# Optimization experiments

Measured on AMD Instinct MI355X. Metric: run time of the kernel, lower is better.

Reference implementation:

```python
import jax, jax.numpy as jnp
import numpy as np

QUERY_DIM = 1024
CONTEXT_DIM = 1024
HEADS = 8
DIM_HEAD = 64
INNER = HEADS * DIM_HEAD  # 512
SCALE = DIM_HEAD ** -0.5


def setup_inputs() -> dict:
    key = jax.random.key(0)
    ks = jax.random.split(key, 7)
    B, N, M = 2, 2048, 2048
    x = jax.random.normal(ks[0], (B, N, QUERY_DIM), dtype=jnp.float32)
    context = jax.random.normal(ks[1], (B, M, CONTEXT_DIM), dtype=jnp.float32)
    # nn.Linear weights (stored as [out, in] in torch; we use [in, out] here)
    Wq = jax.random.normal(ks[2], (QUERY_DIM, INNER), dtype=jnp.float32) * (QUERY_DIM ** -0.5)
    Wk = jax.random.normal(ks[3], (CONTEXT_DIM, INNER), dtype=jnp.float32) * (CONTEXT_DIM ** -0.5)
    Wv = jax.random.normal(ks[4], (CONTEXT_DIM, INNER), dtype=jnp.float32) * (CONTEXT_DIM ** -0.5)
    Wo = jax.random.normal(ks[5], (INNER, QUERY_DIM), dtype=jnp.float32) * (INNER ** -0.5)
    bo = jax.random.normal(ks[6], (QUERY_DIM,), dtype=jnp.float32) * 0.01
    return {"x": x, "context": context, "Wq": Wq, "Wk": Wk, "Wv": Wv, "Wo": Wo, "bo": bo}


def reference(x, context, Wq, Wk, Wv, Wo, bo):
    B, N, _ = x.shape
    M = context.shape[1]
    # projections (no bias, matching nn.Linear(bias=False))
    q = (x @ Wq).reshape(B, N, HEADS, DIM_HEAD)          # b i h d
    k = (context @ Wk).reshape(B, M, HEADS, DIM_HEAD)    # b j h d
    v = (context @ Wv).reshape(B, M, HEADS, DIM_HEAD)    # b j h d
    # scores in fp32 (ATTN_PRECISION=='fp32' path)
    sim = jnp.einsum('bihd,bjhd->bhij', q.astype(jnp.float32), k.astype(jnp.float32)) * SCALE
    attn = jax.nn.softmax(sim, axis=-1).astype(v.dtype)  # b h i j
    out = jnp.einsum('bhij,bjhd->bihd', attn, v).reshape(B, N, INNER)
    return out @ Wo + bo  # dropout p=0.0 is identity
```

## Files before the change

kernel.cpp:

```cpp
#include <hip/hip_runtime.h>
#include <math.h>

typedef __bf16 bf16_t;
typedef __bf16 bf16x8 __attribute__((ext_vector_type(8)));
typedef __bf16 bf16x4 __attribute__((ext_vector_type(4)));
typedef float  f32x4  __attribute__((ext_vector_type(4)));

#define MFMA16(a, b, c) __builtin_amdgcn_mfma_f32_16x16x32_bf16((a), (b), (c), 0, 0, 0)

#define INNER   512
#define DHEAD   64
#define QSCALE  0.18033688f

__device__ __forceinline__ void g2l(const bf16_t* g, bf16_t* l) {
  __builtin_amdgcn_global_load_lds(
      (const __attribute__((address_space(1))) unsigned int*)g,
      (__attribute__((address_space(3))) unsigned int*)l, 16, 0, 0);
}

__global__ __launch_bounds__(256) void cvt_k(const float* __restrict__ x,
                                             const float* __restrict__ ctx,
                                             bf16_t* __restrict__ xb,
                                             bf16_t* __restrict__ cb) {
  const float* in = blockIdx.y ? ctx : x;
  bf16_t* out     = blockIdx.y ? cb  : xb;
  int i = blockIdx.x * 256 + threadIdx.x;
  float4 f = ((const float4*)in)[i];
  bf16x4 v = { (bf16_t)f.x, (bf16_t)f.y, (bf16_t)f.z, (bf16_t)f.w };
  ((bf16x4*)out)[i] = v;
}

__global__ __launch_bounds__(256) void wtrans_k(const float* __restrict__ Wq,
                                                const float* __restrict__ Wk,
                                                const float* __restrict__ Wv,
                                                const float* __restrict__ Wo,
                                                bf16_t* __restrict__ WqT,
                                                bf16_t* __restrict__ WkT,
                                                bf16_t* __restrict__ WvT,
                                                bf16_t* __restrict__ WoT) {
  int z = blockIdx.y;
  const float* W; bf16_t* WT; int K, N;
  if (z == 0)      { W = Wq; WT = WqT; K = 1024; N = 512; }
  else if (z == 1) { W = Wk; WT = WkT; K = 1024; N = 512; }
  else if (z == 2) { W = Wv; WT = WvT; K = 1024; N = 512; }
  else             { W = Wo; WT = WoT; K = 512;  N = 1024; }
  int tK = K >> 6;
  int bid = blockIdx.x;
  int kt = bid % tK, nt = bid / tK;
  int k0 = kt << 6, n0 = nt << 6;
  __shared__ float tile[64][65];
  for (int idx = threadIdx.x; idx < 4096; idx += 256) {
    int r = idx >> 6, c = idx & 63;
    tile[r][c] = W[(size_t)(k0 + r) * N + n0 + c];
  }
  __syncthreads();
  for (int idx = threadIdx.x; idx < 4096; idx += 256) {
    int r = idx >> 6, c = idx & 63;
    WT[(size_t)(n0 + r) * K + k0 + c] = (bf16_t)tile[c][r];
  }
}

__global__ __launch_bounds__(256) void vtrans_k(const bf16_t* __restrict__ Vb,
                                                bf16_t* __restrict__ Vt) {
  int m0 = blockIdx.x << 6;
  int bh = blockIdx.y;
  int b = bh >> 3, h = bh & 7;
  __shared__ bf16_t tile[64][65];
  for (int idx = threadIdx.x; idx < 4096; idx += 256) {
    int r = idx >> 6, c = idx & 63;
    tile[r][c] = Vb[(size_t)(b * 2048 + m0 + r) * INNER + h * DHEAD + c];
  }
  __syncthreads();
  for (int idx = threadIdx.x; idx < 4096; idx += 256) {
    int r = idx >> 6, c = idx & 63;
    Vt[((size_t)bh * 64 + r) * 2048 + m0 + c] = tile[c][r];
  }
}

__device__ __forceinline__ void gemm128(const bf16_t* __restrict__ A,
                                        const bf16_t* __restrict__ Bt,
                                        int K, int N, int row0, int n0, float scale,
                                        bf16_t* __restrict__ Cb, float* __restrict__ Cf,
                                        const float* __restrict__ bias) {
  __shared__ bf16_t As[128 * 40];
  __shared__ bf16_t Bs[128 * 40];
  const int tid = threadIdx.x;
  const int w = tid >> 6, lane = tid & 63, quad = lane >> 4, l16 = lane & 15;
  const int sr = tid >> 2, sc = (tid & 3) << 3;
  const bf16_t* ga = A  + (size_t)(row0 + sr) * K + sc;
  const bf16_t* gb = Bt + (size_t)(n0  + sr) * K + sc;

  f32x4 acc[4][4];
#pragma unroll
  for (int i = 0; i < 4; ++i)
#pragma unroll
    for (int j = 0; j < 4; ++j) acc[i][j] = f32x4{0.f, 0.f, 0.f, 0.f};

  int4 ra0 = *(const int4*)(ga);
  int4 ra1 = *(const int4*)(ga + (size_t)64 * K);
  int4 rb0 = *(const int4*)(gb);
  int4 rb1 = *(const int4*)(gb + (size_t)64 * K);

  const int mrow = (w & 1) << 6, ncol = (w >> 1) << 6;
  const int KT = K >> 5;
  for (int kt = 0; kt < KT; ++kt) {
    __syncthreads();
    *(int4*)&As[sr * 40 + sc]        = ra0;
    *(int4*)&As[(sr + 64) * 40 + sc] = ra1;
    *(int4*)&Bs[sr * 40 + sc]        = rb0;
    *(int4*)&Bs[(sr + 64) * 40 + sc] = rb1;
    __syncthreads();
    if (kt + 1 < KT) {
      int k0 = (kt + 1) << 5;
      ra0 = *(const int4*)(ga + k0);
      ra1 = *(const int4*)(ga + (size_t)64 * K + k0);
      rb0 = *(const int4*)(gb + k0);
      rb1 = *(const int4*)(gb + (size_t)64 * K + k0);
    }
    bf16x8 af[4], bfr[4];
#pragma unroll
    for (int i = 0; i < 4; ++i)
      af[i] = *(const bf16x8*)&As[(mrow + i * 16 + l16) * 40 + quad * 8];
#pragma unroll
    for (int j = 0; j < 4; ++j)
      bfr[j] = *(const bf16x8*)&Bs[(ncol + j * 16 + l16) * 40 + quad * 8];
#pragma unroll
    for (int i = 0; i < 4; ++i)
#pragma unroll
      for (int j = 0; j < 4; ++j)
        acc[i][j] = MFMA16(af[i], bfr[j], acc[i][j]);
  }
#pragma unroll
  for (int i = 0; i < 4; ++i) {
    int row = row0 + mrow + i * 16 + quad * 4;
#pragma unroll
    for (int j = 0; j < 4; ++j) {
      int col = n0 + ncol + j * 16 + l16;
#pragma unroll
      for (int r = 0; r < 4; ++r) {
        if (Cf) Cf[(size_t)(row + r) * N + col] = acc[i][j][r] + bias[col];
        else    Cb[(size_t)(row + r) * N + col] = (bf16_t)(acc[i][j][r] * scale);
      }
    }
  }
}

__global__ __launch_bounds__(256, 2) void gemm_qkv_k(const bf16_t* __restrict__ xb,
                                                     const bf16_t* __restrict__ cb,
                                                     const bf16_t* __restrict__ WqT,
                                                     const bf16_t* __restrict__ WkT,
                                                     const bf16_t* __restrict__ WvT,
                                                     bf16_t* __restrict__ Qb,
                                                     bf16_t* __restrict__ Kb,
                                                     bf16_t* __restrict__ Vb) {
  int z = blockIdx.z;
  const bf16_t* A  = (z == 0) ? xb : cb;
  const bf16_t* Bt = (z == 0) ? WqT : (z == 1) ? WkT : WvT;
  bf16_t* C        = (z == 0) ? Qb  : (z == 1) ? Kb  : Vb;
  float scale      = (z == 0) ? QSCALE : 1.0f;
  gemm128(A, Bt, 1024, 512, blockIdx.y * 128, blockIdx.x * 128, scale, C, nullptr, nullptr);
}

__global__ __launch_bounds__(256, 2) void gemm_out_k(const bf16_t* __restrict__ AO,
                                                     const bf16_t* __restrict__ WoT,
                                                     const float* __restrict__ bo,
                                                     float* __restrict__ out) {
  gemm128(AO, WoT, 512, 1024, blockIdx.y * 128, blockIdx.x * 128, 1.0f, nullptr, out, bo);
}

__global__ __launch_bounds__(256, 3) void attn_k(const bf16_t* __restrict__ Qb,
                                                 const bf16_t* __restrict__ Kb,
                                                 const bf16_t* __restrict__ Vt,
                                                 bf16_t* __restrict__ AO) {
  const int tid = threadIdx.x;
  const int w = tid >> 6, lane = tid & 63, quad = lane >> 4, l16 = lane & 15;
  const int qt = blockIdx.x;
  const int bh = blockIdx.y;
  const int b = bh >> 3, h = bh & 7;

  __shared__ bf16_t KsB[128 * 64];
  __shared__ bf16_t VsB[64 * 128];
  __shared__ bf16_t Ps[64 * 136];

  const int qrow = b * 2048 + qt * 64 + w * 16 + l16;
  const bf16_t* qptr = Qb + (size_t)qrow * INNER + h * DHEAD;
  bf16x8 bq[2];
  bq[0] = *(const bf16x8*)(qptr + quad * 8);
  bq[1] = *(const bf16x8*)(qptr + 32 + quad * 8);

  f32x4 o[4];
#pragma unroll
  for (int dt = 0; dt < 4; ++dt) o[dt] = f32x4{0.f, 0.f, 0.f, 0.f};
  float m_s = -__builtin_inff(), l_s = 0.f;

  const bf16_t* kbase  = Kb + ((size_t)b * 2048) * INNER + h * DHEAD;
  const bf16_t* vtbase = Vt + ((size_t)bh * 64) * 2048;

  const int krow_c = w * 32 + (lane >> 3);
  const int kcol_c = ((lane & 7) ^ (lane >> 3)) << 3;
  const int vrow_c = w * 16 + (lane >> 4);
  bf16_t* ksl = &KsB[w * 2048];
  bf16_t* vsl = &VsB[w * 2048];

  for (int kt = 0; kt < 16; ++kt) {
    __syncthreads();
#pragma unroll
    for (int p = 0; p < 4; ++p) {
      g2l(kbase + (size_t)(kt * 128 + krow_c + p * 8) * INNER + kcol_c,
          ksl + p * 512);
      int vlog = ((lane & 15) ^ ((p * 4 + (lane >> 4)) & 15)) << 3;
      g2l(vtbase + (size_t)(vrow_c + p * 4) * 2048 + kt * 128 + vlog,
          vsl + p * 512);
    }
    __syncthreads();

    f32x4 s[8];
#pragma unroll
    for (int jt = 0; jt < 8; ++jt) s[jt] = f32x4{0.f, 0.f, 0.f, 0.f};
#pragma unroll
    for (int jt = 0; jt < 8; ++jt) {
#pragma unroll
      for (int ks = 0; ks < 2; ++ks) {
        int phys = ((ks * 4 + quad) ^ (l16 & 7)) << 3;
        bf16x8 ak = *(const bf16x8*)&KsB[(jt * 16 + l16) * 64 + phys];
        s[jt] = MFMA16(ak, bq[ks], s[jt]);
      }
    }

    float mx = -__builtin_inff();
#pragma unroll
    for (int jt = 0; jt < 8; ++jt) {
      float a = fmaxf(fmaxf(s[jt][0], s[jt][1]), fmaxf(s[jt][2], s[jt][3]));
      mx = fmaxf(mx, a);
    }
    mx = fmaxf(mx, __shfl_xor(mx, 16, 64));
    mx = fmaxf(mx, __shfl_xor(mx, 32, 64));
    float mnew = fmaxf(m_s, mx);
    float alpha = __builtin_amdgcn_exp2f(m_s - mnew);
    float rs = 0.f;
#pragma unroll
    for (int jt = 0; jt < 8; ++jt) {
#pragma unroll
      for (int r = 0; r < 4; ++r) {
        float p = __builtin_amdgcn_exp2f(s[jt][r] - mnew);
        s[jt][r] = p;
        rs += p;
      }
    }
    rs += __shfl_xor(rs, 16, 64);
    rs += __shfl_xor(rs, 32, 64);
    l_s = l_s * alpha + rs;
    m_s = mnew;
#pragma unroll
    for (int dt = 0; dt < 4; ++dt) o[dt] *= alpha;

#pragma unroll
    for (int jt = 0; jt < 8; ++jt) {
      bf16x4 pk = { (bf16_t)s[jt][0], (bf16_t)s[jt][1],
                    (bf16_t)s[jt][2], (bf16_t)s[jt][3] };
      *(bf16x4*)&Ps[(w * 16 + l16) * 136 + jt * 16 + quad * 4] = pk;
    }

#pragma unroll
    for (int kc = 0; kc < 4; ++kc) {
      bf16x8 bp = *(const bf16x8*)&Ps[(w * 16 + l16) * 136 + kc * 32 + quad * 8];
#pragma unroll
      for (int dt = 0; dt < 4; ++dt) {
        int phys = ((kc * 4 + quad) ^ l16) << 3;
        bf16x8 av = *(const bf16x8*)&VsB[(dt * 16 + l16) * 128 + phys];
        o[dt] = MFMA16(av, bp, o[dt]);
      }
    }
  }

  float inv = 1.0f / l_s;
#pragma unroll
  for (int dt = 0; dt < 4; ++dt) {
    bf16x4 ov = { (bf16_t)(o[dt][0] * inv), (bf16_t)(o[dt][1] * inv),
                  (bf16_t)(o[dt][2] * inv), (bf16_t)(o[dt][3] * inv) };
    *(bf16x4*)&Ps[(w * 16 + l16) * 136 + dt * 16 + quad * 4] = ov;
  }
  __syncthreads();
  {
    int sr = tid >> 2, sc = (tid & 3) << 4;
    int4 r0 = *(const int4*)&Ps[sr * 136 + sc];
    int4 r1 = *(const int4*)&Ps[sr * 136 + sc + 8];
    bf16_t* aout = AO + ((size_t)(b * 2048 + qt * 64 + sr)) * INNER + h * DHEAD + sc;
    *(int4*)aout       = r0;
    *(int4*)(aout + 8) = r1;
  }
}

extern "C" void kernel_launch(void* const* d_in, const int* in_sizes, int n_in,
                              void* d_out, int out_size, void* d_ws, size_t ws_size,
                              hipStream_t stream) {
  const float* x   = (const float*)d_in[0];
  const float* ctx = (const float*)d_in[1];
  const float* Wq  = (const float*)d_in[2];
  const float* Wk  = (const float*)d_in[3];
  const float* Wv  = (const float*)d_in[4];
  const float* Wo  = (const float*)d_in[5];
  const float* bo  = (const float*)d_in[6];
  float* out = (float*)d_out;

  char* ws = (char*)d_ws;
  bf16_t* xb  = (bf16_t*)(ws + 0);
  bf16_t* cb  = (bf16_t*)(ws + 8388608);
  bf16_t* WqT = (bf16_t*)(ws + 16777216);
  bf16_t* WkT = (bf16_t*)(ws + 17825792);
  bf16_t* WvT = (bf16_t*)(ws + 18874368);
  bf16_t* WoT = (bf16_t*)(ws + 19922944);
  bf16_t* Qb  = (bf16_t*)(ws + 20971520);
  bf16_t* Kb  = (bf16_t*)(ws + 25165824);
  bf16_t* Vb  = (bf16_t*)(ws + 29360128);
  bf16_t* Vt  = (bf16_t*)(ws + 33554432);
  bf16_t* AO  = (bf16_t*)(ws + 37748736);

  cvt_k<<<dim3(4096, 2), 256, 0, stream>>>(x, ctx, xb, cb);
  wtrans_k<<<dim3(128, 4), 256, 0, stream>>>(Wq, Wk, Wv, Wo, WqT, WkT, WvT, WoT);
  gemm_qkv_k<<<dim3(4, 32, 3), 256, 0, stream>>>(xb, cb, WqT, WkT, WvT, Qb, Kb, Vb);
  vtrans_k<<<dim3(32, 16), 256, 0, stream>>>(Vb, Vt);
  attn_k<<<dim3(32, 16), 256, 0, stream>>>(Qb, Kb, Vt, AO);
  gemm_out_k<<<dim3(8, 32), 256, 0, stream>>>(AO, WoT, bo, out);
}
```

Measured before the change: 184.7 us.

## Fuse preprocessing kernels, write V transposed from GEMM, double-buffer K in attention

Merges the input-conversion and weight-transpose kernels into one launch and removes the separate V-transpose kernel by having the QKV GEMM epilogue write V directly in transposed per-head layout. The shared GEMM now stages tiles with async global-to-LDS loads and an XOR swizzle instead of register prefetch with padding. The attention kernel double-buffers K tiles and adjusts its barriers, with occupancy bound lowered from 3 to 2. Together these cut launch overhead and extra memory passes, but the GEMM loses its register-prefetch overlap and the transposed V stores are scattered.

```diff
diff --git a/kernel.cpp b/kernel.cpp
--- a/kernel.cpp
+++ b/kernel.cpp
@@ -18,37 +18,39 @@
       (__attribute__((address_space(3))) unsigned int*)l, 16, 0, 0);
 }
 
-__global__ __launch_bounds__(256) void cvt_k(const float* __restrict__ x,
+__global__ __launch_bounds__(256) void pre_k(const float* __restrict__ x,
                                              const float* __restrict__ ctx,
+                                             const float* __restrict__ Wq,
+                                             const float* __restrict__ Wk,
+                                             const float* __restrict__ Wv,
+                                             const float* __restrict__ Wo,
                                              bf16_t* __restrict__ xb,
-                                             bf16_t* __restrict__ cb) {
-  const float* in = blockIdx.y ? ctx : x;
-  bf16_t* out     = blockIdx.y ? cb  : xb;
-  int i = blockIdx.x * 256 + threadIdx.x;
-  float4 f = ((const float4*)in)[i];
-  bf16x4 v = { (bf16_t)f.x, (bf16_t)f.y, (bf16_t)f.z, (bf16_t)f.w };
-  ((bf16x4*)out)[i] = v;
-}
-
-__global__ __launch_bounds__(256) void wtrans_k(const float* __restrict__ Wq,
-                                                const float* __restrict__ Wk,
-                                                const float* __restrict__ Wv,
-                                                const float* __restrict__ Wo,
-                                                bf16_t* __restrict__ WqT,
-                                                bf16_t* __restrict__ WkT,
-                                                bf16_t* __restrict__ WvT,
-                                                bf16_t* __restrict__ WoT) {
-  int z = blockIdx.y;
+                                             bf16_t* __restrict__ cb,
+                                             bf16_t* __restrict__ WqT,
+                                             bf16_t* __restrict__ WkT,
+                                             bf16_t* __restrict__ WvT,
+                                             bf16_t* __restrict__ WoT) {
+  __shared__ float tile[64][65];
+  int bx = blockIdx.x;
+  if (bx < 8192) {
+    const float* in = (bx >= 4096) ? ctx : x;
+    bf16_t* out     = (bx >= 4096) ? cb  : xb;
+    int i = (bx & 4095) * 256 + threadIdx.x;
+    float4 f = ((const float4*)in)[i];
+    bf16x4 v = { (bf16_t)f.x, (bf16_t)f.y, (bf16_t)f.z, (bf16_t)f.w };
+    ((bf16x4*)out)[i] = v;
+    return;
+  }
+  int t = bx - 8192;
+  int z = t >> 7, bid = t & 127;
   const float* W; bf16_t* WT; int K, N;
   if (z == 0)      { W = Wq; WT = WqT; K = 1024; N = 512; }
   else if (z == 1) { W = Wk; WT = WkT; K = 1024; N = 512; }
   else if (z == 2) { W = Wv; WT = WvT; K = 1024; N = 512; }
   else             { W = Wo; WT = WoT; K = 512;  N = 1024; }
   int tK = K >> 6;
-  int bid = blockIdx.x;
   int kt = bid % tK, nt = bid / tK;
   int k0 = kt << 6, n0 = nt << 6;
-  __shared__ float tile[64][65];
   for (int idx = threadIdx.x; idx < 4096; idx += 256) {
     int r = idx >> 6, c = idx & 63;
     tile[r][c] = W[(size_t)(k0 + r) * N + n0 + c];
@@ -60,35 +62,24 @@
   }
 }
 
-__global__ __launch_bounds__(256) void vtrans_k(const bf16_t* __restrict__ Vb,
-                                                bf16_t* __restrict__ Vt) {
-  int m0 = blockIdx.x << 6;
-  int bh = blockIdx.y;
-  int b = bh >> 3, h = bh & 7;
-  __shared__ bf16_t tile[64][65];
-  for (int idx = threadIdx.x; idx < 4096; idx += 256) {
-    int r = idx >> 6, c = idx & 63;
-    tile[r][c] = Vb[(size_t)(b * 2048 + m0 + r) * INNER + h * DHEAD + c];
-  }
-  __syncthreads();
-  for (int idx = threadIdx.x; idx < 4096; idx += 256) {
-    int r = idx >> 6, c = idx & 63;
-    Vt[((size_t)bh * 64 + r) * 2048 + m0 + c] = tile[c][r];
-  }
-}
-
 __device__ __forceinline__ void gemm128(const bf16_t* __restrict__ A,
                                         const bf16_t* __restrict__ Bt,
-                                        int K, int N, int row0, int n0, float scale,
-                                        bf16_t* __restrict__ Cb, float* __restrict__ Cf,
+                                        int K, int N, int row0, int n0,
+                                        int mode, float scale,
+                                        bf16_t* __restrict__ Cb,
+                                        float* __restrict__ Cf,
                                         const float* __restrict__ bias) {
-  __shared__ bf16_t As[128 * 40];
-  __shared__ bf16_t Bs[128 * 40];
+  __shared__ bf16_t As[128 * 32];
+  __shared__ bf16_t Bs[128 * 32];
   const int tid = threadIdx.x;
   const int w = tid >> 6, lane = tid & 63, quad = lane >> 4, l16 = lane & 15;
-  const int sr = tid >> 2, sc = (tid & 3) << 3;
-  const bf16_t* ga = A  + (size_t)(row0 + sr) * K + sc;
-  const bf16_t* gb = Bt + (size_t)(n0  + sr) * K + sc;
+
+  const int srow = lane >> 2;
+  const int logc = (lane & 3) ^ ((lane >> 3) & 3);
+  const bf16_t* gaw = A  + (size_t)(row0 + w * 32 + srow) * K + logc * 8;
+  const bf16_t* gbw = Bt + (size_t)(n0   + w * 32 + srow) * K + logc * 8;
+  bf16_t* lA = As + w * 1024;
+  bf16_t* lB = Bs + w * 1024;
 
   f32x4 acc[4][4];
 #pragma unroll
@@ -96,50 +87,49 @@
 #pragma unroll
     for (int j = 0; j < 4; ++j) acc[i][j] = f32x4{0.f, 0.f, 0.f, 0.f};
 
-  int4 ra0 = *(const int4*)(ga);
-  int4 ra1 = *(const int4*)(ga + (size_t)64 * K);
-  int4 rb0 = *(const int4*)(gb);
-  int4 rb1 = *(const int4*)(gb + (size_t)64 * K);
-
   const int mrow = (w & 1) << 6, ncol = (w >> 1) << 6;
+  const int rphys = (quad ^ ((l16 >> 1) & 3)) << 3;
   const int KT = K >> 5;
-  for (int kt = 0; kt < KT; ++kt) {
+
+  for (int kc = 0; kc < KT; ++kc) {
     __syncthreads();
-    *(int4*)&As[sr * 40 + sc]        = ra0;
-    *(int4*)&As[(sr + 64) * 40 + sc] = ra1;
-    *(int4*)&Bs[sr * 40 + sc]        = rb0;
-    *(int4*)&Bs[(sr + 64) * 40 + sc] = rb1;
+    g2l(gaw + kc * 32,                   lA);
+    g2l(gaw + (size_t)16 * K + kc * 32,  lA + 512);
+    g2l(gbw + kc * 32,                   lB);
+    g2l(gbw + (size_t)16 * K + kc * 32,  lB + 512);
     __syncthreads();
-    if (kt + 1 < KT) {
-      int k0 = (kt + 1) << 5;
-      ra0 = *(const int4*)(ga + k0);
-      ra1 = *(const int4*)(ga + (size_t)64 * K + k0);
-      rb0 = *(const int4*)(gb + k0);
-      rb1 = *(const int4*)(gb + (size_t)64 * K + k0);
-    }
     bf16x8 af[4], bfr[4];
 #pragma unroll
     for (int i = 0; i < 4; ++i)
-      af[i] = *(const bf16x8*)&As[(mrow + i * 16 + l16) * 40 + quad * 8];
+      af[i] = *(const bf16x8*)&As[(mrow + i * 16 + l16) * 32 + rphys];
 #pragma unroll
     for (int j = 0; j < 4; ++j)
-      bfr[j] = *(const bf16x8*)&Bs[(ncol + j * 16 + l16) * 40 + quad * 8];
+      bfr[j] = *(const bf16x8*)&Bs[(ncol + j * 16 + l16) * 32 + rphys];
 #pragma unroll
     for (int i = 0; i < 4; ++i)
 #pragma unroll
       for (int j = 0; j < 4; ++j)
         acc[i][j] = MFMA16(af[i], bfr[j], acc[i][j]);
   }
+
 #pragma unroll
   for (int i = 0; i < 4; ++i) {
     int row = row0 + mrow + i * 16 + quad * 4;
 #pragma unroll
     for (int j = 0; j < 4; ++j) {
       int col = n0 + ncol + j * 16 + l16;
-#pragma unroll
-      for (int r = 0; r < 4; ++r) {
-        if (Cf) Cf[(size_t)(row + r) * N + col] = acc[i][j][r] + bias[col];
-        else    Cb[(size_t)(row + r) * N + col] = (bf16_t)(acc[i][j][r] * scale);
+      if (mode == 2) {
+        int bb = row >> 11, key = row & 2047;
+        int hh = col >> 6,  d   = col & 63;
+        bf16x4 v = { (bf16_t)acc[i][j][0], (bf16_t)acc[i][j][1],
+                     (bf16_t)acc[i][j][2], (bf16_t)acc[i][j][3] };
+        *(bf16x4*)&Cb[((size_t)((bb * 8 + hh) * 64 + d)) * 2048 + key] = v;
+      } else {
+#pragma unroll
+        for (int r = 0; r < 4; ++r) {
+          if (mode == 1) Cf[(size_t)(row + r) * N + col] = acc[i][j][r] + bias[col];
+          else           Cb[(size_t)(row + r) * N + col] = (bf16_t)(acc[i][j][r] * scale);
+        }
       }
     }
   }
@@ -152,23 +142,26 @@
                                                      const bf16_t* __restrict__ WvT,
                                                      bf16_t* __restrict__ Qb,
                                                      bf16_t* __restrict__ Kb,
-                                                     bf16_t* __restrict__ Vb) {
+                                                     bf16_t* __restrict__ Vt) {
   int z = blockIdx.z;
-  const bf16_t* A  = (z == 0) ? xb : cb;
+  const bf16_t* A  = (z == 0) ? xb  : cb;
   const bf16_t* Bt = (z == 0) ? WqT : (z == 1) ? WkT : WvT;
-  bf16_t* C        = (z == 0) ? Qb  : (z == 1) ? Kb  : Vb;
+  bf16_t* C        = (z == 0) ? Qb  : (z == 1) ? Kb  : Vt;
+  int mode         = (z == 2) ? 2 : 0;
   float scale      = (z == 0) ? QSCALE : 1.0f;
-  gemm128(A, Bt, 1024, 512, blockIdx.y * 128, blockIdx.x * 128, scale, C, nullptr, nullptr);
+  gemm128(A, Bt, 1024, 512, blockIdx.y * 128, blockIdx.x * 128, mode, scale,
+          C, nullptr, nullptr);
 }
 
 __global__ __launch_bounds__(256, 2) void gemm_out_k(const bf16_t* __restrict__ AO,
                                                      const bf16_t* __restrict__ WoT,
                                                      const float* __restrict__ bo,
                                                      float* __restrict__ out) {
-  gemm128(AO, WoT, 512, 1024, blockIdx.y * 128, blockIdx.x * 128, 1.0f, nullptr, out, bo);
-}
-
-__global__ __launch_bounds__(256, 3) void attn_k(const bf16_t* __restrict__ Qb,
+  gemm128(AO, WoT, 512, 1024, blockIdx.y * 128, blockIdx.x * 128, 1, 1.0f,
+          nullptr, out, bo);
+}
+
+__global__ __launch_bounds__(256, 2) void attn_k(const bf16_t* __restrict__ Qb,
                                                  const bf16_t* __restrict__ Kb,
                                                  const bf16_t* __restrict__ Vt,
                                                  bf16_t* __restrict__ AO) {
@@ -178,8 +171,8 @@
   const int bh = blockIdx.y;
   const int b = bh >> 3, h = bh & 7;
 
-  __shared__ bf16_t KsB[128 * 64];
-  __shared__ bf16_t VsB[64 * 128];
+  __shared__ bf16_t Ks[2 * 128 * 64];
+  __shared__ bf16_t Vs[64 * 128];
   __shared__ bf16_t Ps[64 * 136];
 
   const int qrow = b * 2048 + qt * 64 + w * 16 + l16;
@@ -196,23 +189,30 @@
   const bf16_t* kbase  = Kb + ((size_t)b * 2048) * INNER + h * DHEAD;
   const bf16_t* vtbase = Vt + ((size_t)bh * 64) * 2048;
 
-  const int krow_c = w * 32 + (lane >> 3);
-  const int kcol_c = ((lane & 7) ^ (lane >> 3)) << 3;
-  const int vrow_c = w * 16 + (lane >> 4);
-  bf16_t* ksl = &KsB[w * 2048];
-  bf16_t* vsl = &VsB[w * 2048];
+  const int krow = lane >> 3;
+  const int kcol = ((lane & 7) ^ (lane >> 3)) << 3;
+  const int vrow = lane >> 4;
+
+#pragma unroll
+  for (int p = 0; p < 4; ++p)
+    g2l(kbase + (size_t)(w * 32 + p * 8 + krow) * INNER + kcol,
+        &Ks[w * 2048 + p * 512]);
 
   for (int kt = 0; kt < 16; ++kt) {
+    const int cur = (kt & 1) * 8192, nxt = ((kt + 1) & 1) * 8192;
     __syncthreads();
+    if (kt < 16 - 1) {
+#pragma unroll
+      for (int p = 0; p < 4; ++p)
+        g2l(kbase + (size_t)((kt + 1) * 128 + w * 32 + p * 8 + krow) * INNER + kcol,
+            &Ks[nxt + w * 2048 + p * 512]);
+    }
 #pragma unroll
     for (int p = 0; p < 4; ++p) {
-      g2l(kbase + (size_t)(kt * 128 + krow_c + p * 8) * INNER + kcol_c,
-          ksl + p * 512);
-      int vlog = ((lane & 15) ^ ((p * 4 + (lane >> 4)) & 15)) << 3;
-      g2l(vtbase + (size_t)(vrow_c + p * 4) * 2048 + kt * 128 + vlog,
-          vsl + p * 512);
-    }
-    __syncthreads();
+      int vlog = ((lane & 15) ^ ((p * 4 + vrow) & 15)) << 3;
+      g2l(vtbase + (size_t)(w * 16 + p * 4 + vrow) * 2048 + kt * 128 + vlog,
+          &Vs[w * 2048 + p * 512]);
+    }
 
     f32x4 s[8];
 #pragma unroll
@@ -222,7 +222,7 @@
 #pragma unroll
       for (int ks = 0; ks < 2; ++ks) {
         int phys = ((ks * 4 + quad) ^ (l16 & 7)) << 3;
-        bf16x8 ak = *(const bf16x8*)&KsB[(jt * 16 + l16) * 64 + phys];
+        bf16x8 ak = *(const bf16x8*)&Ks[cur + (jt * 16 + l16) * 64 + phys];
         s[jt] = MFMA16(ak, bq[ks], s[jt]);
       }
     }
@@ -261,13 +261,15 @@
       *(bf16x4*)&Ps[(w * 16 + l16) * 136 + jt * 16 + quad * 4] = pk;
     }
 
+    __syncthreads();
+
 #pragma unroll
     for (int kc = 0; kc < 4; ++kc) {
       bf16x8 bp = *(const bf16x8*)&Ps[(w * 16 + l16) * 136 + kc * 32 + quad * 8];
 #pragma unroll
       for (int dt = 0; dt < 4; ++dt) {
         int phys = ((kc * 4 + quad) ^ l16) << 3;
-        bf16x8 av = *(const bf16x8*)&VsB[(dt * 16 + l16) * 128 + phys];
+        bf16x8 av = *(const bf16x8*)&Vs[(dt * 16 + l16) * 128 + phys];
         o[dt] = MFMA16(av, bp, o[dt]);
       }
     }
@@ -304,22 +306,20 @@
   float* out = (float*)d_out;
 
   char* ws = (char*)d_ws;
-  bf16_t* xb  = (bf16_t*)(ws + 0);
-  bf16_t* cb  = (bf16_t*)(ws + 8388608);
-  bf16_t* WqT = (bf16_t*)(ws + 16777216);
-  bf16_t* WkT = (bf16_t*)(ws + 17825792);
-  bf16_t* WvT = (bf16_t*)(ws + 18874368);
-  bf16_t* WoT = (bf16_t*)(ws + 19922944);
-  bf16_t* Qb  = (bf16_t*)(ws + 20971520);
-  bf16_t* Kb  = (bf16_t*)(ws + 25165824);
-  bf16_t* Vb  = (bf16_t*)(ws + 29360128);
-  bf16_t* Vt  = (bf16_t*)(ws + 33554432);
-  bf16_t* AO  = (bf16_t*)(ws + 37748736);
-
-  cvt_k<<<dim3(4096, 2), 256, 0, stream>>>(x, ctx, xb, cb);
-  wtrans_k<<<dim3(128, 4), 256, 0, stream>>>(Wq, Wk, Wv, Wo, WqT, WkT, WvT, WoT);
-  gemm_qkv_k<<<dim3(4, 32, 3), 256, 0, stream>>>(xb, cb, WqT, WkT, WvT, Qb, Kb, Vb);
-  vtrans_k<<<dim3(32, 16), 256, 0, stream>>>(Vb, Vt);
+  const size_t MB = 1048576;
+  bf16_t* xb  = (bf16_t*)(ws + 0 * MB);
+  bf16_t* cb  = (bf16_t*)(ws + 8 * MB);
+  bf16_t* WqT = (bf16_t*)(ws + 16 * MB);
+  bf16_t* WkT = (bf16_t*)(ws + 17 * MB);
+  bf16_t* WvT = (bf16_t*)(ws + 18 * MB);
+  bf16_t* WoT = (bf16_t*)(ws + 19 * MB);
+  bf16_t* Qb  = (bf16_t*)(ws + 20 * MB);
+  bf16_t* Kb  = (bf16_t*)(ws + 24 * MB);
+  bf16_t* Vt  = (bf16_t*)(ws + 28 * MB);
+  bf16_t* AO  = (bf16_t*)(ws + 32 * MB);
+
+  pre_k<<<8704, 256, 0, stream>>>(x, ctx, Wq, Wk, Wv, Wo, xb, cb, WqT, WkT, WvT, WoT);
+  gemm_qkv_k<<<dim3(4, 32, 3), 256, 0, stream>>>(xb, cb, WqT, WkT, WvT, Qb, Kb, Vt);
   attn_k<<<dim3(32, 16), 256, 0, stream>>>(Qb, Kb, Vt, AO);
   gemm_out_k<<<dim3(8, 32), 256, 0, stream>>>(AO, WoT, bo, out);
 }
```

After: 172.1 us. -6.8%, faster.
